# Performance work log

Hardware: AMD Instinct MI355X
Metric: run time of the kernel (lower is better)

## Reference

```python
import jax, jax.numpy as jnp
import numpy as np

D_MODEL = 2048
D_INNER = 4096      # expand * d_model
HEADDIM = 64
NHEADS = 64         # d_inner // headdim
D_STATE = 128
NGROUPS = 1
D_CONV = 4
CHUNK = 128
EPS = 1e-5
BATCH = 2
SEQLEN = 4096
D_CONV_CH = D_INNER + 2 * NGROUPS * D_STATE            # 4352
D_IN_PROJ = 2 * D_INNER + 2 * NGROUPS * D_STATE + NHEADS  # 8512


def setup_inputs() -> dict:
    ks = jax.random.split(jax.random.key(0), 9)
    u = jax.random.normal(ks[0], (BATCH, SEQLEN, D_MODEL), jnp.float32)
    W_in = jax.random.normal(ks[1], (D_MODEL, D_IN_PROJ), jnp.float32) * 0.02
    conv_w = jax.random.normal(ks[2], (D_CONV_CH, D_CONV), jnp.float32) * 0.2
    conv_b = jax.random.normal(ks[3], (D_CONV_CH,), jnp.float32) * 0.02
    dt_bias = jax.random.normal(ks[4], (NHEADS,), jnp.float32) * 0.1
    A_log = jax.random.normal(ks[5], (NHEADS,), jnp.float32) * 0.1
    D = jnp.ones((NHEADS,), jnp.float32)
    norm_w = jnp.ones((D_INNER,), jnp.float32)
    W_out = jax.random.normal(ks[8], (D_INNER, D_MODEL), jnp.float32) * 0.02
    return dict(u=u, W_in=W_in, conv_w=conv_w, conv_b=conv_b, dt_bias=dt_bias,
                A_log=A_log, D=D, norm_w=norm_w, W_out=W_out)


def _mamba2_forward(u, W_in, conv_w, conv_b, dt_bias, A_log, D, norm_w, W_out):
    b, L, _ = u.shape
    zxbcdt = u @ W_in                                       # (b, L, 8512)
    z = zxbcdt[..., :D_INNER]
    xBC = zxbcdt[..., D_INNER:D_INNER + D_CONV_CH]
    dt = zxbcdt[..., D_INNER + D_CONV_CH:]                  # (b, L, h)

    # causal depthwise conv1d (padding = d_conv-1, truncated to L) + SiLU
    padded = jnp.pad(xBC, ((0, 0), (D_CONV - 1, 0), (0, 0)))
    xBC_conv = conv_b + sum(padded[:, k:k + L, :] * conv_w[:, k] for k in range(D_CONV))
    xBC_act = jax.nn.silu(xBC_conv)

    x = xBC_act[..., :D_INNER].reshape(b, L, NHEADS, HEADDIM)
    Bm = xBC_act[..., D_INNER:D_INNER + NGROUPS * D_STATE].reshape(b, L, NGROUPS, D_STATE)
    Cm = xBC_act[..., D_INNER + NGROUPS * D_STATE:].reshape(b, L, NGROUPS, D_STATE)
    rep = NHEADS // NGROUPS
    Bh = jnp.repeat(Bm, rep, axis=2)                        # (b, L, h, n)
    Ch = jnp.repeat(Cm, rep, axis=2)

    A = -jnp.exp(A_log)                                     # (h,), negative
    dtf = jax.nn.softplus(dt + dt_bias)                     # (b, L, h)

    # ---- chunked SSD (structured state-space duality) scan ----
    nc = L // CHUNK
    xc = x.reshape(b, nc, CHUNK, NHEADS, HEADDIM)
    Bc = Bh.reshape(b, nc, CHUNK, NHEADS, D_STATE)
    Cc = Ch.reshape(b, nc, CHUNK, NHEADS, D_STATE)
    dtc = dtf.reshape(b, nc, CHUNK, NHEADS)
    cum = jnp.cumsum(dtc * A, axis=2)                       # (b, nc, cs, h), decreasing

    # intra-chunk causal decay matrix L_ij = exp(cum_i - cum_j), i >= j
    idx = jnp.arange(CHUNK)
    mask = (idx[:, None] >= idx[None, :])[None, None, :, :, None]
    seg = cum[:, :, :, None, :] - cum[:, :, None, :, :]     # (b, nc, i, j, h)
    decay = jnp.exp(jnp.where(mask, seg, -jnp.inf))
    CB = jnp.einsum('bcihn,bcjhn->bcijh', Cc, Bc)
    Y_diag = jnp.einsum('bcijh,bcjh,bcjhp->bcihp', CB * decay, dtc, xc)

    # per-chunk final states: sum_j exp(cum_last - cum_j) * dt_j * B_j (x) x_j
    decay_last = jnp.exp(cum[:, :, -1:, :] - cum)           # (b, nc, cs, h)
    states = jnp.einsum('bclh,bclhn,bclhp->bchpn', decay_last * dtc, Bc, xc)

    # inter-chunk recurrence: carry_{c+1} = exp(sum dA_c) * carry_c + states_c
    Atot = jnp.exp(cum[:, :, -1, :])                        # (b, nc, h)
    def step(carry, inp):
        a, s = inp
        return a[..., None, None] * carry + s, carry
    init = jnp.zeros((b, NHEADS, HEADDIM, D_STATE), jnp.float32)
    _, prev = jax.lax.scan(step, init, (jnp.moveaxis(Atot, 1, 0), jnp.moveaxis(states, 1, 0)))
    prev = jnp.moveaxis(prev, 0, 1)                         # (b, nc, h, p, n) state entering each chunk

    Y_off = jnp.einsum('bclhn,bclh,bchpn->bclhp', Cc, jnp.exp(cum), prev)

    y = (Y_diag + Y_off).reshape(b, L, NHEADS, HEADDIM) + D[:, None] * x
    y = y.reshape(b, L, D_INNER)

    # gated RMSNorm: rmsnorm(y * silu(z)) * norm_w
    t = y * jax.nn.silu(z)
    t = t * jax.lax.rsqrt(jnp.mean(t * t, axis=-1, keepdims=True) + EPS) * norm_w
    return t @ W_out


def reference(u, W_in, conv_w, conv_b, dt_bias, A_log, D, norm_w, W_out):
    return _mamba2_forward(u, W_in, conv_w, conv_b, dt_bias, A_log, D, norm_w, W_out)
```

## Files before the change

kernel.cpp:

```cpp
#include <hip/hip_runtime.h>

#define BATCH 2
#define SEQLEN 4096
#define DM 2048
#define DIP 8512
#define DIPP 8576
#define DI 4096
#define DCC 4352
#define NH 64
#define HD 64
#define DSZ 128
#define CHK 128
#define NC 32
#define NBL (BATCH*SEQLEN)
#define LDP 136

typedef __attribute__((ext_vector_type(4))) float f32x4;
typedef __attribute__((ext_vector_type(8))) __bf16 bf16x8;
typedef __attribute__((ext_vector_type(8))) unsigned short us8;
typedef __attribute__((ext_vector_type(4))) unsigned short us4;

__device__ inline float bf2f(unsigned short u){ union{unsigned int i; float f;} v; v.i=((unsigned)u)<<16; return v.f; }
__device__ inline unsigned short f2bf(float f){ union{float f; unsigned int i;} v; v.f=f; unsigned r=(v.i + 0x7FFFu + ((v.i>>16)&1u))>>16; return (unsigned short)r; }

#define GLOAD_LDS16(gp, lp) __builtin_amdgcn_global_load_lds( \
    (const __attribute__((address_space(1))) void*)(gp), \
    (__attribute__((address_space(3))) void*)(lp), 16, 0, 0)

__global__ void beacon_kernel(float* __restrict__ out, float v)
{
    if (blockIdx.x == 0 && threadIdx.x == 0) out[0] = v;
}

__global__ void cast_bf16_kernel(const float* __restrict__ src, unsigned short* __restrict__ dst, size_t n)
{
    size_t stride = (size_t)gridDim.x * blockDim.x * 8;
    for (size_t i = ((size_t)blockIdx.x*blockDim.x + threadIdx.x)*8; i < n; i += stride) {
        float4 a = *(const float4*)&src[i];
        float4 b = *(const float4*)&src[i+4];
        us8 o;
        o[0]=f2bf(a.x); o[1]=f2bf(a.y); o[2]=f2bf(a.z); o[3]=f2bf(a.w);
        o[4]=f2bf(b.x); o[5]=f2bf(b.y); o[6]=f2bf(b.z); o[7]=f2bf(b.w);
        *(us8*)&dst[i] = o;
    }
}

__global__ __launch_bounds__(256) void transpose_cast_kernel(
    const float* __restrict__ in, unsigned short* __restrict__ out, int R, int C)
{
    __shared__ float tile[32][33];
    const int c0 = blockIdx.x*32, r0 = blockIdx.y*32;
    const int tx = threadIdx.x & 31, ty = threadIdx.x >> 5;
    #pragma unroll
    for (int i = 0; i < 4; i++) {
        const int r = r0 + ty + i*8;
        const int c = c0 + tx;
        tile[ty+i*8][tx] = (c < C) ? in[(size_t)r*C + c] : 0.f;
    }
    __syncthreads();
    #pragma unroll
    for (int i = 0; i < 4; i++) {
        const int cc = c0 + ty + i*8;
        const int rr = r0 + tx;
        out[(size_t)cc*R + rr] = f2bf(tile[tx][ty+i*8]);
    }
}

template<int EPI>
__global__ __launch_bounds__(512, 2) void gemm256(
    const unsigned short* __restrict__ A, const unsigned short* __restrict__ Bt,
    float* __restrict__ C, int K, int ldc, int Nmax,
    unsigned short* __restrict__ zbf, unsigned short* __restrict__ xbcbf,
    float* __restrict__ dtf, const float* __restrict__ dt_bias)
{
    __shared__ unsigned short L[65536];
    const int m0 = blockIdx.x * 256;
    const int n0 = blockIdx.y * 256;
    const int tid = threadIdx.x;
    const int lane = tid & 63;
    const int wid  = tid >> 6;
    const int wm = wid >> 2, wn = wid & 3;
    const int lr  = lane & 15;
    const int lkg = (lane >> 4) * 8;
    const int srow = (wid << 4) + (lane >> 3);
    const int scol = ((lane & 7) ^ (lane >> 3)) << 3;
    const int cs0 = lkg ^ ((lr & 7) << 3);
    const int cs1 = cs0 ^ 32;
    const int nt = K >> 6;

    f32x4 acc[8][4];
    #pragma unroll
    for (int i=0;i<8;i++)
        #pragma unroll
        for (int j=0;j<4;j++) acc[i][j] = f32x4{0.f,0.f,0.f,0.f};

    auto stA = [&](int buf, int t, int h) {
        const unsigned short* g = A + (size_t)(m0 + h*128 + srow)*K + t*64 + scol;
        GLOAD_LDS16(g,               &L[buf*32768 + h*8192 + wid*1024]);
        GLOAD_LDS16(g + (size_t)8*K, &L[buf*32768 + h*8192 + wid*1024 + 512]);
    };
    auto stB = [&](int buf, int t, int h) {
        const int rr = n0 + h*128 + srow;
        const int r0 = (rr     > Nmax) ? Nmax : rr;
        const int r1 = (rr + 8 > Nmax) ? Nmax : rr + 8;
        GLOAD_LDS16(Bt + (size_t)r0*K + t*64 + scol, &L[buf*32768 + 16384 + h*8192 + wid*1024]);
        GLOAD_LDS16(Bt + (size_t)r1*K + t*64 + scol, &L[buf*32768 + 16384 + h*8192 + wid*1024 + 512]);
    };

    bf16x8 bfr[4][2];
    auto rdA = [&](int buf, int mq, int s, int ks) {
        const int rl = mq*32 + s*16 + lr;
        return *(const bf16x8*)&L[buf*32768 + wm*8192 + rl*64 + (ks ? cs1 : cs0)];
    };
    auto rdB = [&](int buf, int nf, int ks) {
        const int rl = (wn & 1)*64 + nf*16 + lr;
        return *(const bf16x8*)&L[buf*32768 + 16384 + (wn >> 1)*8192 + rl*64 + (ks ? cs1 : cs0)];
    };

#define PH(BUF, MQ, LOADB, ...) do { \
    bf16x8 af[2][2]; \
    af[0][0]=rdA(BUF,MQ,0,0); af[0][1]=rdA(BUF,MQ,0,1); \
    af[1][0]=rdA(BUF,MQ,1,0); af[1][1]=rdA(BUF,MQ,1,1); \
    if (LOADB) { \
        _Pragma("unroll") \
        for (int nf=0;nf<4;nf++){ bfr[nf][0]=rdB(BUF,nf,0); bfr[nf][1]=rdB(BUF,nf,1);} } \
    __VA_ARGS__; \
    asm volatile("s_barrier" ::: "memory"); \
    __builtin_amdgcn_s_setprio(1); \
    _Pragma("unroll") \
    for (int s=0;s<2;s++) { \
        _Pragma("unroll") \
        for (int nf=0;nf<4;nf++) { \
            acc[MQ*2+s][nf] = __builtin_amdgcn_mfma_f32_16x16x32_bf16(af[s][0], bfr[nf][0], acc[MQ*2+s][nf], 0,0,0); \
            acc[MQ*2+s][nf] = __builtin_amdgcn_mfma_f32_16x16x32_bf16(af[s][1], bfr[nf][1], acc[MQ*2+s][nf], 0,0,0); } } \
    __builtin_amdgcn_s_setprio(0); \
    asm volatile("s_barrier" ::: "memory"); \
} while(0)

    stA(0, 0, 0); stA(0, 0, 1); stB(0, 0, 0); stB(0, 0, 1);
    stB(1, 1, 0); stB(1, 1, 1);
    asm volatile("s_waitcnt vmcnt(4)" ::: "memory");
    asm volatile("s_barrier" ::: "memory");

    #pragma unroll 1
    for (int t = 0; t < nt; t += 2) {
        const int tp2 = (t + 2 < nt) ? t + 2 : nt - 1;
        const int tp3 = (t + 3 < nt) ? t + 3 : nt - 1;
        PH(0, 0, true,  stA(1, t+1, 0));
        PH(0, 1, false, stA(1, t+1, 1); stB(0, tp2, 0));
        PH(0, 2, false, stB(0, tp2, 1));
        PH(0, 3, false, asm volatile("s_waitcnt vmcnt(4)" ::: "memory"));
        PH(1, 0, true,  stA(0, tp2, 0));
        PH(1, 1, false, stA(0, tp2, 1); stB(1, tp3, 0));
        PH(1, 2, false, stB(1, tp3, 1));
        PH(1, 3, false, asm volatile("s_waitcnt vmcnt(4)" ::: "memory"));
    }
#undef PH

    const int cr = (lane >> 4) * 4;
    const int cc = lane & 15;
    #pragma unroll
    for (int i=0;i<8;i++) {
        #pragma unroll
        for (int j=0;j<4;j++) {
            const int row = m0 + wm*128 + i*16 + cr;
            const int col = n0 + wn*64 + j*16 + cc;
            #pragma unroll
            for (int r=0;r<4;r++) {
                const float val = acc[i][j][r];
                const int rr = row + r;
                if (EPI == 0) {
                    C[(size_t)rr*ldc + col] = val;
                } else {
                    if (col < DI) {
                        zbf[(size_t)rr*DI + col] = f2bf(val);
                    } else if (col < DI + DCC) {
                        xbcbf[(size_t)rr*DCC + (col - DI)] = f2bf(val);
                    } else if (col < DI + DCC + NH) {
                        const int hh = col - (DI + DCC);
                        const float x = val + dt_bias[hh];
                        dtf[(size_t)rr*NH + hh] = (x > 20.f) ? x : log1pf(__expf(x));
                    }
                }
            }
        }
    }
}

__global__ __launch_bounds__(256) void conv_x_kernel(
    const unsigned short* __restrict__ xbc,
    const float* __restrict__ cw, const float* __restrict__ cb,
    unsigned short* __restrict__ xT)
{
    __shared__ float raw[67][68];
    __shared__ unsigned short ot[64][72];
    const int lt = blockIdx.x;
    const int h  = blockIdx.y;
    const int b  = lt >> 6;
    const int l0 = (lt & 63) * 64;
    const int t = threadIdx.x;

    for (int i = t; i < 536; i += 256) {
        const int li = i >> 3, cg = (i & 7) * 8;
        const int l = l0 - 3 + li;
        us8 v;
        #pragma unroll
        for (int e = 0; e < 8; e++) v[e] = 0;
        if (l >= 0) v = *(const us8*)&xbc[(size_t)(b*SEQLEN + l)*DCC + h*64 + cg];
        #pragma unroll
        for (int e = 0; e < 8; e++) raw[li][cg+e] = bf2f(v[e]);
    }
    __syncthreads();
    #pragma unroll
    for (int j = 0; j < 16; j++) {
        const int i = t + j*256;
        const int l = i >> 6, p = i & 63;
        const int ch = h*64 + p;
        float a = cb[ch];
        #pragma unroll
        for (int k = 0; k < 4; k++) a += raw[l + k][p] * cw[ch*4 + k];
        a = a / (1.f + __expf(-a));
        ot[l][p] = f2bf(a);
    }
    __syncthreads();
    for (int i = t; i < 512; i += 256) {
        const int p = i >> 3, lg = (i & 7) * 8;
        us8 o;
        #pragma unroll
        for (int e = 0; e < 8; e++) o[e] = ot[lg + e][p];
        *(us8*)&xT[(size_t)((b*NH + h)*HD + p)*SEQLEN + l0 + lg] = o;
    }
}

__global__ void conv_bc_kernel(const unsigned short* __restrict__ xbc,
                               const float* __restrict__ cw, const float* __restrict__ cb,
                               unsigned short* __restrict__ bcbf)
{
    const int idx = blockIdx.x*256 + threadIdx.x;
    if (idx >= NBL*32) return;
    const int g = idx & 31;
    const int row = idx >> 5;
    const int l = row & (SEQLEN-1);
    const int ch0 = DI + g*8;
    float a[8];
    #pragma unroll
    for (int e=0;e<8;e++) a[e] = cb[ch0+e];
    #pragma unroll
    for (int k = 0; k < 4; k++) {
        if (l + k >= 3) {
            us8 v = *(const us8*)&xbc[(size_t)(row + k - 3)*DCC + ch0];
            #pragma unroll
            for (int e=0;e<8;e++) a[e] += bf2f(v[e]) * cw[(ch0+e)*4 + k];
        }
    }
    us8 o;
    #pragma unroll
    for (int e=0;e<8;e++){ const float s = a[e]/(1.f+__expf(-a[e])); o[e]=f2bf(s); }
    *(us8*)&bcbf[(size_t)row*256 + g*8] = o;
}

__global__ void cum_kernel(const float* __restrict__ dtf, const float* __restrict__ A_log,
                           float* __restrict__ cum)
{
    const int idx = blockIdx.x*256 + threadIdx.x;
    const int h = idx & 63;
    const int bc = idx >> 6;
    const float A = -__expf(A_log[h]);
    float c = 0.f;
    const float* src = dtf + (size_t)bc*CHK*NH + h;
    float* dst = cum + (size_t)bc*CHK*NH + h;
    for (int i = 0; i < CHK; i++) { c += src[i*NH]*A; dst[i*NH] = c; }
}

__global__ __launch_bounds__(256) void ssm_passS(
    const unsigned short* __restrict__ bcbf,
    const unsigned short* __restrict__ xT,
    const float* __restrict__ cumg,
    const float* __restrict__ dtfg,
    unsigned short* __restrict__ states)
{
    __shared__ unsigned short BT[128*LDP];
    __shared__ unsigned short XW[64*LDP];
    __shared__ float cum_s[128], dtc_s[128], w_s[128];

    const int blk = blockIdx.x;
    const int h = blk & 63;
    const int bc = blk >> 6;
    const int r0 = bc * CHK;
    const int t = threadIdx.x;
    const int lane = t & 63;
    const int wid = t >> 6;

    if (t < 128) {
        cum_s[t] = cumg[(size_t)(r0+t)*NH + h];
        dtc_s[t] = dtfg[(size_t)(r0+t)*NH + h];
    }
    for (int i = t; i < 2048; i += 256) {
        const int l = i >> 4, cg = (i & 15)*8;
        us8 v = *(const us8*)(bcbf + (size_t)(r0+l)*256 + cg);
        #pragma unroll
        for (int e = 0; e < 8; e++) BT[(cg+e)*LDP + l] = v[e];
    }
    __syncthreads();
    if (t < 128) w_s[t] = __expf(cum_s[127] - cum_s[t]) * dtc_s[t];
    __syncthreads();
    {
        const int b = bc >> 5;
        const int li = (bc & 31) * CHK;
        const unsigned short* xb = xT + (size_t)((b*NH + h)*HD)*SEQLEN + li;
        for (int i = t; i < 1024; i += 256) {
            const int p = i >> 4, cg = (i & 15)*8;
            us8 v = *(const us8*)(xb + (size_t)p*SEQLEN + cg);
            #pragma unroll
            for (int e = 0; e < 8; e++) v[e] = f2bf(bf2f(v[e]) * w_s[cg+e]);
            *(us8*)&XW[p*LDP + cg] = v;
        }
    }
    __syncthreads();

    const int lr = lane & 15;
    const int lkg = (lane >> 4)*8;
    const int wr = wid >> 1, wc = wid & 1;

    f32x4 acc[2][4];
    #pragma unroll
    for (int i=0;i<2;i++)
        #pragma unroll
        for (int j=0;j<4;j++) acc[i][j] = f32x4{0.f,0.f,0.f,0.f};
    #pragma unroll
    for (int k = 0; k < 4; k++) {
        bf16x8 a[2], b[4];
        #pragma unroll
        for (int i=0;i<2;i++) a[i] = *(const bf16x8*)&XW[(wr*32 + i*16 + lr)*LDP + k*32 + lkg];
        #pragma unroll
        for (int j=0;j<4;j++) b[j] = *(const bf16x8*)&BT[(wc*64 + j*16 + lr)*LDP + k*32 + lkg];
        #pragma unroll
        for (int i=0;i<2;i++)
            #pragma unroll
            for (int j=0;j<4;j++)
                acc[i][j] = __builtin_amdgcn_mfma_f32_16x16x32_bf16(a[i], b[j], acc[i][j], 0,0,0);
    }
    unsigned short* sb = states + (size_t)blk * (HD*DSZ);
    const int cr = (lane >> 4)*4, cc = lane & 15;
    #pragma unroll
    for (int i=0;i<2;i++) {
        #pragma unroll
        for (int j=0;j<4;j++) {
            const int nn = wc*64 + j*16 + cc;
            #pragma unroll
            for (int r=0;r<4;r++) {
                const int pp = wr*32 + i*16 + cr + r;
                sb[pp*DSZ + nn] = f2bf(acc[i][j][r]);
            }
        }
    }
}

__global__ void scan_kernel(unsigned short* __restrict__ states, const float* __restrict__ cumg)
{
    const int idx = blockIdx.x*256 + threadIdx.x;
    const int n = idx & 127;
    const int p = (idx >> 7) & 63;
    const int h = (idx >> 13) & 63;
    const int b = idx >> 19;
    float carry = 0.f;
    for (int c = 0; c < NC; c++) {
        const size_t off = ((size_t)((b*NC + c)*NH + h))*(HD*DSZ) + p*DSZ + n;
        const float s = bf2f(states[off]);
        states[off] = f2bf(carry);
        const float atot = __expf(cumg[(size_t)((b*NC+c)*CHK + 127)*NH + h]);
        carry = atot*carry + s;
    }
}

__global__ __launch_bounds__(256) void ssm_passY(
    const unsigned short* __restrict__ bcbf,
    const unsigned short* __restrict__ xT,
    const unsigned short* __restrict__ statesg,
    const float* __restrict__ cumg,
    const float* __restrict__ dtfg,
    const float* __restrict__ Dg,
    unsigned short* __restrict__ y)
{
    __shared__ unsigned short P1[128*LDP];
    __shared__ unsigned short P2[128*LDP];
    __shared__ unsigned short XTs[64*LDP];
    __shared__ unsigned short PV[64*LDP];
    __shared__ float cum_s[128], dtc_s[128];

    const int blk = blockIdx.x;
    const int h = blk & 63;
    const int bc = blk >> 6;
    const int r0 = bc * CHK;
    const int t = threadIdx.x;
    const int lane = t & 63;
    const int wid = t >> 6;

    if (t < 128) {
        cum_s[t] = cumg[(size_t)(r0+t)*NH + h];
        dtc_s[t] = dtfg[(size_t)(r0+t)*NH + h];
    }
    for (int i = t; i < 2048; i += 256) {
        const int l = i >> 4, cg = (i & 15)*8;
        const unsigned short* src = bcbf + (size_t)(r0+l)*256 + cg;
        *(us8*)&P2[l*LDP + cg] = *(const us8*)src;
        *(us8*)&P1[l*LDP + cg] = *(const us8*)(src + 128);
    }
    {
        const int b = bc >> 5;
        const int li = (bc & 31) * CHK;
        const unsigned short* xb = xT + (size_t)((b*NH + h)*HD)*SEQLEN + li;
        const unsigned short* sb = statesg + (size_t)blk * (HD*DSZ);
        for (int i = t; i < 1024; i += 256) {
            const int p = i >> 4, cg = (i & 15)*8;
            *(us8*)&XTs[p*LDP + cg] = *(const us8*)(xb + (size_t)p*SEQLEN + cg);
            *(us8*)&PV[p*LDP + cg]  = *(const us8*)(sb + p*DSZ + cg);
        }
    }
    __syncthreads();

    const int lr = lane & 15;
    const int lkg = (lane >> 4)*8;
    const int wr = wid >> 1, wc = wid & 1;

    f32x4 acc1[4][4], acc2[4][2];
    #pragma unroll
    for (int i=0;i<4;i++) {
        #pragma unroll
        for (int j=0;j<4;j++) acc1[i][j] = f32x4{0.f,0.f,0.f,0.f};
        #pragma unroll
        for (int j=0;j<2;j++) acc2[i][j] = f32x4{0.f,0.f,0.f,0.f};
    }
    #pragma unroll
    for (int k = 0; k < 4; k++) {
        bf16x8 a[4], b[4], pv[2];
        #pragma unroll
        for (int i=0;i<4;i++) a[i] = *(const bf16x8*)&P1[(wr*64 + i*16 + lr)*LDP + k*32 + lkg];
        #pragma unroll
        for (int j=0;j<4;j++) b[j] = *(const bf16x8*)&P2[(wc*64 + j*16 + lr)*LDP + k*32 + lkg];
        #pragma unroll
        for (int j=0;j<2;j++) pv[j] = *(const bf16x8*)&PV[(wc*32 + j*16 + lr)*LDP + k*32 + lkg];
        #pragma unroll
        for (int i=0;i<4;i++) {
            #pragma unroll
            for (int j=0;j<4;j++)
                acc1[i][j] = __builtin_amdgcn_mfma_f32_16x16x32_bf16(a[i], b[j], acc1[i][j], 0,0,0);
            #pragma unroll
            for (int j=0;j<2;j++)
                acc2[i][j] = __builtin_amdgcn_mfma_f32_16x16x32_bf16(a[i], pv[j], acc2[i][j], 0,0,0);
        }
    }
    __syncthreads();
    const int cr = (lane >> 4)*4, cc = lane & 15;
    #pragma unroll
    for (int i=0;i<4;i++) {
        #pragma unroll
        for (int j=0;j<4;j++) {
            const int jj = wc*64 + j*16 + cc;
            #pragma unroll
            for (int r=0;r<4;r++) {
                const int ii = wr*64 + i*16 + cr + r;
                float v = 0.f;
                if (jj <= ii) v = acc1[i][j][r] * __expf(cum_s[ii] - cum_s[jj]) * dtc_s[jj];
                P1[ii*LDP + jj] = f2bf(v);
            }
        }
    }
    __syncthreads();
    #pragma unroll
    for (int i=0;i<4;i++) {
        #pragma unroll
        for (int r=0;r<4;r++) {
            const int ii = wr*64 + i*16 + cr + r;
            const float sc = __expf(cum_s[ii]);
            #pragma unroll
            for (int j=0;j<2;j++) acc2[i][j][r] *= sc;
        }
    }
    #pragma unroll
    for (int k = 0; k < 4; k++) {
        bf16x8 a[4], x2[2];
        #pragma unroll
        for (int i=0;i<4;i++) a[i] = *(const bf16x8*)&P1[(wr*64 + i*16 + lr)*LDP + k*32 + lkg];
        #pragma unroll
        for (int j=0;j<2;j++) x2[j] = *(const bf16x8*)&XTs[(wc*32 + j*16 + lr)*LDP + k*32 + lkg];
        #pragma unroll
        for (int i=0;i<4;i++)
            #pragma unroll
            for (int j=0;j<2;j++)
                acc2[i][j] = __builtin_amdgcn_mfma_f32_16x16x32_bf16(a[i], x2[j], acc2[i][j], 0,0,0);
    }
    const float Dv = Dg[h];
    #pragma unroll
    for (int i=0;i<4;i++) {
        #pragma unroll
        for (int j=0;j<2;j++) {
            const int pp = wc*32 + j*16 + cc;
            #pragma unroll
            for (int r=0;r<4;r++) {
                const int ii = wr*64 + i*16 + cr + r;
                const float xv = bf2f(XTs[pp*LDP + ii]);
                y[(size_t)(r0+ii)*DI + h*64 + pp] = f2bf(acc2[i][j][r] + Dv * xv);
            }
        }
    }
}

__global__ __launch_bounds__(256) void gate_rms_kernel(
    const unsigned short* __restrict__ y, const unsigned short* __restrict__ z,
    const float* __restrict__ nw, unsigned short* __restrict__ tbf)
{
    const int row = blockIdx.x;
    const int t = threadIdx.x;
    const int lane = t & 63, wid = t >> 6;
    float tv[16];
    float ss = 0.f;
    #pragma unroll
    for (int i = 0; i < 2; i++) {
        const int c = (i*256 + t)*8;
        const us8 yv = *(const us8*)&y[(size_t)row*DI + c];
        const us8 zv = *(const us8*)&z[(size_t)row*DI + c];
        #pragma unroll
        for (int e = 0; e < 8; e++) {
            const float fy = bf2f(yv[e]);
            const float fz = bf2f(zv[e]);
            const float v = fy * (fz / (1.f + __expf(-fz)));
            tv[i*8+e] = v;
            ss += v*v;
        }
    }
    #pragma unroll
    for (int o = 1; o < 64; o <<= 1) ss += __shfl_xor(ss, o, 64);
    __shared__ float red[4];
    if (lane == 0) red[wid] = ss;
    __syncthreads();
    const float rms = rsqrtf((red[0]+red[1]+red[2]+red[3]) * (1.f/DI) + 1e-5f);
    #pragma unroll
    for (int i = 0; i < 2; i++) {
        const int c = (i*256 + t)*8;
        us8 o;
        #pragma unroll
        for (int e = 0; e < 8; e += 4) {
            const float4 wv = *(const float4*)&nw[c + e];
            o[e+0]=f2bf(tv[i*8+e+0]*rms*wv.x);
            o[e+1]=f2bf(tv[i*8+e+1]*rms*wv.y);
            o[e+2]=f2bf(tv[i*8+e+2]*rms*wv.z);
            o[e+3]=f2bf(tv[i*8+e+3]*rms*wv.w);
        }
        *(us8*)&tbf[(size_t)row*DI + c] = o;
    }
}

extern "C" void kernel_launch(void* const* d_in, const int* in_sizes, int n_in,
                              void* d_out, int out_size, void* d_ws, size_t ws_size,
                              hipStream_t stream)
{
    const float* u       = (const float*)d_in[0];
    const float* W_in    = (const float*)d_in[1];
    const float* conv_w  = (const float*)d_in[2];
    const float* conv_b  = (const float*)d_in[3];
    const float* dt_bias = (const float*)d_in[4];
    const float* A_log   = (const float*)d_in[5];
    const float* Dp      = (const float*)d_in[6];
    const float* norm_w  = (const float*)d_in[7];
    const float* W_out   = (const float*)d_in[8];
    float* out = (float*)d_out;

    char* ws = (char*)d_ws;
    const size_t OFF_WINT = 33554432;
    const size_t OFF_R2   = 68681728;
    const size_t OFF_R3   = 139984896;
    const size_t OFF_SM   = 207093760;
    const size_t NEED     = OFF_SM + 2097152 + 2097152 + 4194304;
    if (ws_size < NEED) {
        beacon_kernel<<<1, 64, 0, stream>>>(out, 10000.f + (float)(ws_size >> 20));
        return;
    }

    unsigned short* u_bf   = (unsigned short*)(ws);
    unsigned short* winT   = (unsigned short*)(ws + OFF_WINT);
    unsigned short* xTb    = (unsigned short*)(ws);
    unsigned short* t_bf   = (unsigned short*)(ws);
    unsigned short* xbc_bf = (unsigned short*)(ws + OFF_R2);
    unsigned short* y_bf   = (unsigned short*)(ws + OFF_R2);
    unsigned short* states = (unsigned short*)(ws + OFF_R3);
    unsigned short* woutT  = (unsigned short*)(ws + OFF_R3);
    float*          dtf    = (float*)(ws + OFF_SM);
    float*          cum    = (float*)(ws + OFF_SM + 2097152);
    unsigned short* bc_bf  = (unsigned short*)(ws + OFF_SM + 4194304);
    unsigned short* z_bf   = (unsigned short*)d_out;

    cast_bf16_kernel<<<2048, 256, 0, stream>>>(u, u_bf, (size_t)NBL*DM);
    transpose_cast_kernel<<<dim3(DIPP/32, DM/32), 256, 0, stream>>>(W_in, winT, DM, DIP);
    gemm256<1><<<dim3(NBL/256, (DIPP+255)/256), 512, 0, stream>>>(
        u_bf, winT, nullptr, DM, 0, DIPP-1, z_bf, xbc_bf, dtf, dt_bias);
    conv_x_kernel<<<dim3(NBL/64, NH), 256, 0, stream>>>(xbc_bf, conv_w, conv_b, xTb);
    conv_bc_kernel<<<(NBL*32)/256, 256, 0, stream>>>(xbc_bf, conv_w, conv_b, bc_bf);
    cum_kernel<<<16, 256, 0, stream>>>(dtf, A_log, cum);
    ssm_passS<<<BATCH*NC*NH, 256, 0, stream>>>(bc_bf, xTb, cum, dtf, states);
    scan_kernel<<<4096, 256, 0, stream>>>(states, cum);
    ssm_passY<<<BATCH*NC*NH, 256, 0, stream>>>(bc_bf, xTb, states, cum, dtf, Dp, y_bf);
    gate_rms_kernel<<<NBL, 256, 0, stream>>>(y_bf, z_bf, norm_w, t_bf);
    transpose_cast_kernel<<<dim3(DM/32, DI/32), 256, 0, stream>>>(W_out, woutT, DI, DM);
    gemm256<0><<<dim3(NBL/256, DM/256), 512, 0, stream>>>(
        t_bf, woutT, out, DI, DM, DM-1, nullptr, nullptr, nullptr, nullptr);
}
```

Measured before the change: 958.2 us.

## Software-pipeline LDS fragment reads ahead of MFMA phases in GEMM; spread cum kernel

The GEMM main loop now double-buffers the A and B register fragments, so each phase reads the next quarter's LDS fragments before running the MFMAs on the current ones. This hides LDS read latency behind matrix work instead of reading and then computing in sequence. It costs more VGPRs, which could lower occupancy or cause spills, and it changes the tail clamp for tp2. Separately, the cumulative-sum kernel is launched with 64 blocks of 64 threads instead of 16 blocks of 256, spreading its serial work over more CUs.

```diff
diff --git a/kernel.cpp b/kernel.cpp
--- a/kernel.cpp
+++ b/kernel.cpp
@@ -106,8 +106,6 @@
         GLOAD_LDS16(Bt + (size_t)r0*K + t*64 + scol, &L[buf*32768 + 16384 + h*8192 + wid*1024]);
         GLOAD_LDS16(Bt + (size_t)r1*K + t*64 + scol, &L[buf*32768 + 16384 + h*8192 + wid*1024 + 512]);
     };
-
-    bf16x8 bfr[4][2];
     auto rdA = [&](int buf, int mq, int s, int ks) {
         const int rl = mq*32 + s*16 + lr;
         return *(const bf16x8*)&L[buf*32768 + wm*8192 + rl*64 + (ks ? cs1 : cs0)];
@@ -117,45 +115,61 @@
         return *(const bf16x8*)&L[buf*32768 + 16384 + (wn >> 1)*8192 + rl*64 + (ks ? cs1 : cs0)];
     };
 
-#define PH(BUF, MQ, LOADB, ...) do { \
-    bf16x8 af[2][2]; \
-    af[0][0]=rdA(BUF,MQ,0,0); af[0][1]=rdA(BUF,MQ,0,1); \
-    af[1][0]=rdA(BUF,MQ,1,0); af[1][1]=rdA(BUF,MQ,1,1); \
-    if (LOADB) { \
-        _Pragma("unroll") \
-        for (int nf=0;nf<4;nf++){ bfr[nf][0]=rdB(BUF,nf,0); bfr[nf][1]=rdB(BUF,nf,1);} } \
-    __VA_ARGS__; \
-    asm volatile("s_barrier" ::: "memory"); \
+#define BAR asm volatile("s_barrier" ::: "memory")
+#define VM4 asm volatile("s_waitcnt vmcnt(4)" ::: "memory")
+#define RD_A(AF, BUF, MQ) do { \
+    AF[0][0]=rdA(BUF,MQ,0,0); AF[0][1]=rdA(BUF,MQ,0,1); \
+    AF[1][0]=rdA(BUF,MQ,1,0); AF[1][1]=rdA(BUF,MQ,1,1); } while(0)
+#define RD_B(BF, BUF) do { \
+    _Pragma("unroll") \
+    for (int nf=0;nf<4;nf++){ BF[nf][0]=rdB(BUF,nf,0); BF[nf][1]=rdB(BUF,nf,1);} } while(0)
+#define MFMA_Q(MQ, AF, BF) do { \
     __builtin_amdgcn_s_setprio(1); \
     _Pragma("unroll") \
     for (int s=0;s<2;s++) { \
         _Pragma("unroll") \
         for (int nf=0;nf<4;nf++) { \
-            acc[MQ*2+s][nf] = __builtin_amdgcn_mfma_f32_16x16x32_bf16(af[s][0], bfr[nf][0], acc[MQ*2+s][nf], 0,0,0); \
-            acc[MQ*2+s][nf] = __builtin_amdgcn_mfma_f32_16x16x32_bf16(af[s][1], bfr[nf][1], acc[MQ*2+s][nf], 0,0,0); } } \
+            acc[(MQ)*2+s][nf] = __builtin_amdgcn_mfma_f32_16x16x32_bf16(AF[s][0], BF[nf][0], acc[(MQ)*2+s][nf], 0,0,0); \
+            acc[(MQ)*2+s][nf] = __builtin_amdgcn_mfma_f32_16x16x32_bf16(AF[s][1], BF[nf][1], acc[(MQ)*2+s][nf], 0,0,0); } } \
     __builtin_amdgcn_s_setprio(0); \
-    asm volatile("s_barrier" ::: "memory"); \
 } while(0)
 
     stA(0, 0, 0); stA(0, 0, 1); stB(0, 0, 0); stB(0, 0, 1);
     stB(1, 1, 0); stB(1, 1, 1);
-    asm volatile("s_waitcnt vmcnt(4)" ::: "memory");
-    asm volatile("s_barrier" ::: "memory");
+    VM4;
+    BAR;
+    bf16x8 afA[2][2], afB[2][2], bfA[4][2], bfB[4][2];
+    RD_A(afA, 0, 0);
+    RD_B(bfA, 0);
 
     #pragma unroll 1
     for (int t = 0; t < nt; t += 2) {
-        const int tp2 = (t + 2 < nt) ? t + 2 : nt - 1;
+        const int tp2 = (t + 2 < nt) ? t + 2 : nt - 2;
         const int tp3 = (t + 3 < nt) ? t + 3 : nt - 1;
-        PH(0, 0, true,  stA(1, t+1, 0));
-        PH(0, 1, false, stA(1, t+1, 1); stB(0, tp2, 0));
-        PH(0, 2, false, stB(0, tp2, 1));
-        PH(0, 3, false, asm volatile("s_waitcnt vmcnt(4)" ::: "memory"));
-        PH(1, 0, true,  stA(0, tp2, 0));
-        PH(1, 1, false, stA(0, tp2, 1); stB(1, tp3, 0));
-        PH(1, 2, false, stB(1, tp3, 1));
-        PH(1, 3, false, asm volatile("s_waitcnt vmcnt(4)" ::: "memory"));
-    }
-#undef PH
+        RD_A(afB, 0, 1); stA(1, t+1, 0);
+        BAR; MFMA_Q(0, afA, bfA); BAR;
+        RD_A(afA, 0, 2); stA(1, t+1, 1); stB(0, tp2, 0);
+        BAR; MFMA_Q(1, afB, bfA); BAR;
+        RD_A(afB, 0, 3); stB(0, tp2, 1);
+        VM4;
+        BAR; MFMA_Q(2, afA, bfA); BAR;
+        RD_A(afA, 1, 0); RD_B(bfB, 1);
+        BAR; MFMA_Q(3, afB, bfA); BAR;
+        RD_A(afB, 1, 1); stA(0, tp2, 0);
+        BAR; MFMA_Q(0, afA, bfB); BAR;
+        RD_A(afA, 1, 2); stA(0, tp2, 1); stB(1, tp3, 0);
+        BAR; MFMA_Q(1, afB, bfB); BAR;
+        RD_A(afB, 1, 3); stB(1, tp3, 1);
+        VM4;
+        BAR; MFMA_Q(2, afA, bfB); BAR;
+        RD_A(afA, 0, 0); RD_B(bfA, 0);
+        BAR; MFMA_Q(3, afB, bfB); BAR;
+    }
+#undef BAR
+#undef VM4
+#undef RD_A
+#undef RD_B
+#undef MFMA_Q
 
     const int cr = (lane >> 4) * 4;
     const int cc = lane & 15;
@@ -262,7 +276,8 @@
 __global__ void cum_kernel(const float* __restrict__ dtf, const float* __restrict__ A_log,
                            float* __restrict__ cum)
 {
-    const int idx = blockIdx.x*256 + threadIdx.x;
+    const int idx = blockIdx.x*blockDim.x + threadIdx.x;
+    if (idx >= BATCH*NC*NH) return;
     const int h = idx & 63;
     const int bc = idx >> 6;
     const float A = -__expf(A_log[h]);
@@ -596,7 +611,7 @@
         u_bf, winT, nullptr, DM, 0, DIPP-1, z_bf, xbc_bf, dtf, dt_bias);
     conv_x_kernel<<<dim3(NBL/64, NH), 256, 0, stream>>>(xbc_bf, conv_w, conv_b, xTb);
     conv_bc_kernel<<<(NBL*32)/256, 256, 0, stream>>>(xbc_bf, conv_w, conv_b, bc_bf);
-    cum_kernel<<<16, 256, 0, stream>>>(dtf, A_log, cum);
+    cum_kernel<<<64, 64, 0, stream>>>(dtf, A_log, cum);
     ssm_passS<<<BATCH*NC*NH, 256, 0, stream>>>(bc_bf, xTb, cum, dtf, states);
     scan_kernel<<<4096, 256, 0, stream>>>(states, cum);
     ssm_passY<<<BATCH*NC*NH, 256, 0, stream>>>(bc_bf, xTb, states, cum, dtf, Dp, y_bf);
```

Measured after the change: 988.5 us. 1.03x slower.
